# Performance work log

Hardware: AMD Instinct MI355X
Metric: run time of the kernel (lower is better)

The kernel has to match this reference:

```python
import jax, jax.numpy as jnp
from jax import lax
import numpy as np

NUM_CLASSES = 85742  # MS1M-scale classifier
C = 512              # feature channels
KH = KW = 1          # 1x1 conv classifier kernel
B = 512              # batch size
H = W = 7            # feature map spatial size


def setup_inputs() -> dict:
    key = jax.random.key(0)
    kx, kw = jax.random.split(key)
    x = jax.random.normal(kx, (B, C, H, W), dtype=jnp.float32)
    # labels: all distinct so torch's labels.unique() has deterministic size B
    labels = jnp.arange(B, dtype=jnp.int64)
    weight = jax.random.normal(kw, (NUM_CLASSES, C, KH, KW), dtype=jnp.float32) * 0.02
    bias = jnp.zeros((NUM_CLASSES,), dtype=jnp.float32)  # requires_grad=False in torch
    return {"x": x, "labels": labels, "weight": weight, "bias": bias}


def reference(x, labels, weight, bias):
    # Partial-FC style: gather the unique-label subset of the classifier weight,
    # then run a conv producing logits only over that subset.
    # jnp.unique with static size=B is jit-compatible; labels are all distinct here.
    labels_unique = jnp.unique(labels, size=labels.shape[0], fill_value=0)  # [U], sorted
    w_sub = weight[labels_unique]   # [U, C, KH, KW] irregular gather
    b_sub = bias[labels_unique]     # [U]
    logits = lax.conv_general_dilated(
        x, w_sub,
        window_strides=(1, 1), padding="VALID",
        dimension_numbers=("NCHW", "OIHW", "NCHW"),
    )  # [B, U, H, W]
    return logits + b_sub[None, :, None, None]
```

## Files before the change

kernel.cpp:

```cpp
#include <hip/hip_runtime.h>
#include <hip/hip_bf16.h>

#define CIN    512
#define BATCH  512
#define HW     49
#define UDIM   512
#define MTOT   (BATCH * HW)
#define MT     128
#define NMB    (MTOT / MT)
#define UHALF  256
#define KT     16
#define NSTEP  (CIN / KT)
#define NBLK   (NMB * 2)

typedef short  bf16x8 __attribute__((ext_vector_type(8)));
typedef short  s16x4  __attribute__((ext_vector_type(4)));
typedef float  f32x16 __attribute__((ext_vector_type(16)));

#define MFMA32(A, B, C) __builtin_amdgcn_mfma_f32_32x32x16_bf16((A), (B), (C), 0, 0, 0)

__device__ __forceinline__ void gload_lds16(const void* g, void* l) {
  __builtin_amdgcn_global_load_lds(
      (const __attribute__((address_space(1))) void*)g,
      (__attribute__((address_space(3))) void*)l, 16, 0, 0);
}

__device__ __forceinline__ void split2(float v, unsigned short& h, unsigned short& l) {
  unsigned int b  = __float_as_uint(v);
  unsigned int hb = (b + 0x7FFFu + ((b >> 16) & 1u)) >> 16;
  float hf        = __uint_as_float(hb << 16);
  unsigned int lb = __float_as_uint(v - hf);
  h = (unsigned short)hb;
  l = (unsigned short)((lb + 0x7FFFu + ((lb >> 16) & 1u)) >> 16);
}

__device__ __forceinline__ f32x16 zero16() {
  f32x16 r;
#pragma unroll
  for (int i = 0; i < 16; ++i) r[i] = 0.f;
  return r;
}

__global__ void sort_gather(const int* __restrict__ labels,
                            const float* __restrict__ bias,
                            int* __restrict__ sorted,
                            float* __restrict__ bsub)
{
  __shared__ int sl[BATCH];
  const int i = threadIdx.x;
  const int stride = (labels[1] == 0) ? 2 : 1;
  const int li = labels[i * stride];
  sl[i] = li;
  __syncthreads();
  int rank = 0;
#pragma unroll 8
  for (int j = 0; j < BATCH; ++j) rank += (sl[j] < li) ? 1 : 0;
  sorted[rank] = li;
  bsub[rank]   = bias[li];
}

__global__ void wprep(const float* __restrict__ weight,
                      const int* __restrict__ sorted,
                      unsigned short* __restrict__ whi,
                      unsigned short* __restrict__ wlo)
{
  const int u   = blockIdx.x;
  const int lbl = sorted[u];
  const float* wrow = weight + (size_t)lbl * CIN;
  for (int k = threadIdx.x; k < CIN; k += 256) {
    unsigned short h, l;
    split2(wrow[k], h, l);
    const int s = k >> 4, kq = (k >> 3) & 1, j = k & 7;
    const size_t idx = (((size_t)(s * 2 + kq)) * UDIM + u) * 8 + j;
    whi[idx] = h;
    wlo[idx] = l;
  }
}

__global__ __launch_bounds__(512, 4) void convcls_main(
    const float* __restrict__ x,
    const unsigned short* __restrict__ whi,
    const unsigned short* __restrict__ wlo,
    const float* __restrict__ bsub,
    float* __restrict__ out)
{
  __shared__ __attribute__((aligned(16))) unsigned short WhB[2][2][UHALF][8];
  __shared__ __attribute__((aligned(16))) unsigned short WlB[2][2][UHALF][8];
  __shared__ __attribute__((aligned(16))) unsigned short XhB[2][2][MT][8];
  __shared__ __attribute__((aligned(16))) unsigned short XlB[2][2][MT][8];

  const int bid = blockIdx.x;
  const int swz = (bid & 7) * (NBLK / 8) + (bid >> 3);
  const int uh  = swz / NMB;
  const int mb  = swz - uh * NMB;

  const int tid  = threadIdx.x;
  const int wave = tid >> 6, lane = tid & 63;
  const int l31  = lane & 31, lq = lane >> 5;

  const int mloc = tid & 127;
  const int ks   = tid >> 7;
  const int kqs  = ks >> 1;
  const int j0   = (ks & 1) * 4;
  const int mg   = mb * MT + mloc;
  const int bimg = mg / HW;
  const int hwp  = mg - bimg * HW;
  const float* xsrc = x + (size_t)bimg * (CIN * HW) + hwp;

  const size_t wsrcbase =
      ((size_t)(wave >> 2) * UDIM + uh * UHALF + (wave & 3) * 64) * 8 + lane * 8;

  f32x16 a00 = zero16(), a01 = zero16(), a10 = zero16(), a11 = zero16();

  const int uoff = (wave & 3) * 64;
  const int moff = (wave >> 2) * 64;

  {
    float v[4];
#pragma unroll
    for (int i = 0; i < 4; ++i) v[i] = xsrc[(size_t)(ks * 4 + i) * HW];
    gload_lds16(whi + wsrcbase, (char*)&WhB[0][0][0][0] + wave * 1024);
    gload_lds16(wlo + wsrcbase, (char*)&WlB[0][0][0][0] + wave * 1024);
    s16x4 ph, pl;
#pragma unroll
    for (int i = 0; i < 4; ++i) {
      unsigned short h, l; split2(v[i], h, l);
      ph[i] = (short)h; pl[i] = (short)l;
    }
    *(s16x4*)&XhB[0][kqs][mloc][j0] = ph;
    *(s16x4*)&XlB[0][kqs][mloc][j0] = pl;
  }
  __syncthreads();

  for (int s = 0; s < NSTEP; ++s) {
    const int cur = s & 1, nxt = cur ^ 1;
    const bool pf = (s + 1 < NSTEP);
    float v[4];
    if (pf) {
      const size_t so = (size_t)(s + 1) * (2 * UDIM * 8);
      gload_lds16(whi + so + wsrcbase, (char*)&WhB[nxt][0][0][0] + wave * 1024);
      gload_lds16(wlo + so + wsrcbase, (char*)&WlB[nxt][0][0][0] + wave * 1024);
#pragma unroll
      for (int i = 0; i < 4; ++i)
        v[i] = xsrc[(size_t)((s + 1) * KT + ks * 4 + i) * HW];
    }

    bf16x8 ah0 = *(const bf16x8*)&WhB[cur][lq][uoff + l31][0];
    bf16x8 ah1 = *(const bf16x8*)&WhB[cur][lq][uoff + 32 + l31][0];
    bf16x8 al0 = *(const bf16x8*)&WlB[cur][lq][uoff + l31][0];
    bf16x8 al1 = *(const bf16x8*)&WlB[cur][lq][uoff + 32 + l31][0];
    bf16x8 bh0 = *(const bf16x8*)&XhB[cur][lq][moff + l31][0];
    bf16x8 bh1 = *(const bf16x8*)&XhB[cur][lq][moff + 32 + l31][0];
    bf16x8 bl0 = *(const bf16x8*)&XlB[cur][lq][moff + l31][0];
    bf16x8 bl1 = *(const bf16x8*)&XlB[cur][lq][moff + 32 + l31][0];

    a00 = MFMA32(ah0, bh0, a00);  a01 = MFMA32(ah0, bh1, a01);
    a10 = MFMA32(ah1, bh0, a10);  a11 = MFMA32(ah1, bh1, a11);
    a00 = MFMA32(ah0, bl0, a00);  a01 = MFMA32(ah0, bl1, a01);
    a10 = MFMA32(ah1, bl0, a10);  a11 = MFMA32(ah1, bl1, a11);
    a00 = MFMA32(al0, bh0, a00);  a01 = MFMA32(al0, bh1, a01);
    a10 = MFMA32(al1, bh0, a10);  a11 = MFMA32(al1, bh1, a11);

    if (pf) {
      s16x4 ph, pl;
#pragma unroll
      for (int i = 0; i < 4; ++i) {
        unsigned short h, l; split2(v[i], h, l);
        ph[i] = (short)h; pl[i] = (short)l;
      }
      *(s16x4*)&XhB[nxt][kqs][mloc][j0] = ph;
      *(s16x4*)&XlB[nxt][kqs][mloc][j0] = pl;
    }
    __syncthreads();
  }

  const int u0g = uh * UHALF + uoff;
  const int m0g = mb * MT + moff;
  const int mA  = m0g + l31,      mB = m0g + 32 + l31;
  const int bA  = mA / HW,        hA = mA - bA * HW;
  const int bB  = mB / HW,        hB = mB - bB * HW;
  float* oA = out + (size_t)bA * (UDIM * HW) + hA;
  float* oB = out + (size_t)bB * (UDIM * HW) + hB;
#pragma unroll
  for (int r = 0; r < 16; ++r) {
    const int urow = (r & 3) + 8 * (r >> 2) + 4 * lq;
    {
      const int u = u0g + urow;
      const float bs = bsub[u];
      oA[(size_t)u * HW] = a00[r] + bs;
      oB[(size_t)u * HW] = a01[r] + bs;
    }
    {
      const int u = u0g + 32 + urow;
      const float bs = bsub[u];
      oA[(size_t)u * HW] = a10[r] + bs;
      oB[(size_t)u * HW] = a11[r] + bs;
    }
  }
}

extern "C" void kernel_launch(void* const* d_in, const int* in_sizes, int n_in,
                              void* d_out, int out_size, void* d_ws, size_t ws_size,
                              hipStream_t stream)
{
  const float* x      = (const float*)d_in[0];
  const int*   labels = (const int*)d_in[1];
  const float* weight = (const float*)d_in[2];
  const float* bias   = (const float*)d_in[3];
  float*       out    = (float*)d_out;

  int*            sorted = (int*)d_ws;
  float*          bsub   = (float*)((char*)d_ws + 2048);
  unsigned short* whi    = (unsigned short*)((char*)d_ws + 4096);
  unsigned short* wlo    = (unsigned short*)((char*)d_ws + 4096 + 512 * 1024);

  sort_gather<<<1, BATCH, 0, stream>>>(labels, bias, sorted, bsub);
  wprep<<<UDIM, 256, 0, stream>>>(weight, sorted, whi, wlo);
  convcls_main<<<NBLK, 512, 0, stream>>>(x, whi, wlo, bsub, out);
}
```

Measured before the change: 314.0 us.

## Fuse label sort, weight gather and split into main conv kernel

Removes the separate sort and weight-prep kernels. Each block now ranks the labels itself, gathers its half of the weight rows straight from global memory, and splits them into bf16 hi/lo inside the main loop. This saves two launches and the round trip of the prepared weights through the workspace. In exchange, every block repeats the 512x512 rank computation and the hi/lo conversion of the weights, and uses plain vector loads instead of direct-to-LDS loads.

```diff
diff --git a/kernel.cpp b/kernel.cpp
--- a/kernel.cpp
+++ b/kernel.cpp
@@ -15,15 +15,11 @@
 
 typedef short  bf16x8 __attribute__((ext_vector_type(8)));
 typedef short  s16x4  __attribute__((ext_vector_type(4)));
+typedef short  s16x8  __attribute__((ext_vector_type(8)));
+typedef float  f32x4  __attribute__((ext_vector_type(4)));
 typedef float  f32x16 __attribute__((ext_vector_type(16)));
 
 #define MFMA32(A, B, C) __builtin_amdgcn_mfma_f32_32x32x16_bf16((A), (B), (C), 0, 0, 0)
-
-__device__ __forceinline__ void gload_lds16(const void* g, void* l) {
-  __builtin_amdgcn_global_load_lds(
-      (const __attribute__((address_space(1))) void*)g,
-      (__attribute__((address_space(3))) void*)l, 16, 0, 0);
-}
 
 __device__ __forceinline__ void split2(float v, unsigned short& h, unsigned short& l) {
   unsigned int b  = __float_as_uint(v);
@@ -41,53 +37,20 @@
   return r;
 }
 
-__global__ void sort_gather(const int* __restrict__ labels,
-                            const float* __restrict__ bias,
-                            int* __restrict__ sorted,
-                            float* __restrict__ bsub)
-{
-  __shared__ int sl[BATCH];
-  const int i = threadIdx.x;
-  const int stride = (labels[1] == 0) ? 2 : 1;
-  const int li = labels[i * stride];
-  sl[i] = li;
-  __syncthreads();
-  int rank = 0;
-#pragma unroll 8
-  for (int j = 0; j < BATCH; ++j) rank += (sl[j] < li) ? 1 : 0;
-  sorted[rank] = li;
-  bsub[rank]   = bias[li];
-}
-
-__global__ void wprep(const float* __restrict__ weight,
-                      const int* __restrict__ sorted,
-                      unsigned short* __restrict__ whi,
-                      unsigned short* __restrict__ wlo)
-{
-  const int u   = blockIdx.x;
-  const int lbl = sorted[u];
-  const float* wrow = weight + (size_t)lbl * CIN;
-  for (int k = threadIdx.x; k < CIN; k += 256) {
-    unsigned short h, l;
-    split2(wrow[k], h, l);
-    const int s = k >> 4, kq = (k >> 3) & 1, j = k & 7;
-    const size_t idx = (((size_t)(s * 2 + kq)) * UDIM + u) * 8 + j;
-    whi[idx] = h;
-    wlo[idx] = l;
-  }
-}
-
-__global__ __launch_bounds__(512, 4) void convcls_main(
+__global__ __launch_bounds__(512, 4) void convcls_fused(
     const float* __restrict__ x,
-    const unsigned short* __restrict__ whi,
-    const unsigned short* __restrict__ wlo,
-    const float* __restrict__ bsub,
-    float* __restrict__ out)
+    const int*   __restrict__ labels,
+    const float* __restrict__ weight,
+    const float* __restrict__ bias,
+    float*       __restrict__ out)
 {
   __shared__ __attribute__((aligned(16))) unsigned short WhB[2][2][UHALF][8];
   __shared__ __attribute__((aligned(16))) unsigned short WlB[2][2][UHALF][8];
   __shared__ __attribute__((aligned(16))) unsigned short XhB[2][2][MT][8];
   __shared__ __attribute__((aligned(16))) unsigned short XlB[2][2][MT][8];
+  __shared__ int   sl[BATCH];
+  __shared__ int   lblr[UHALF];
+  __shared__ float bsubs[UHALF];
 
   const int bid = blockIdx.x;
   const int swz = (bid & 7) * (NBLK / 8) + (bid >> 3);
@@ -98,6 +61,22 @@
   const int wave = tid >> 6, lane = tid & 63;
   const int l31  = lane & 31, lq = lane >> 5;
 
+  {
+    const int stride = (labels[1] == 0) ? 2 : 1;
+    const int lt = labels[tid * stride];
+    sl[tid] = lt;
+    __syncthreads();
+    int rank = 0;
+#pragma unroll 8
+    for (int j = 0; j < BATCH; ++j) rank += (sl[j] < lt) ? 1 : 0;
+    const int rloc = rank - uh * UHALF;
+    if ((unsigned)rloc < UHALF) { lblr[rloc] = lt; bsubs[rloc] = bias[lt]; }
+    __syncthreads();
+  }
+
+  const int uloc = tid & 255;
+  const int kq   = tid >> 8;
+  const float* wp = weight + (size_t)lblr[uloc] * CIN + kq * 8;
   const int mloc = tid & 127;
   const int ks   = tid >> 7;
   const int kqs  = ks >> 1;
@@ -107,42 +86,48 @@
   const int hwp  = mg - bimg * HW;
   const float* xsrc = x + (size_t)bimg * (CIN * HW) + hwp;
 
-  const size_t wsrcbase =
-      ((size_t)(wave >> 2) * UDIM + uh * UHALF + (wave & 3) * 64) * 8 + lane * 8;
-
   f32x16 a00 = zero16(), a01 = zero16(), a10 = zero16(), a11 = zero16();
-
   const int uoff = (wave & 3) * 64;
   const int moff = (wave >> 2) * 64;
 
   {
-    float v[4];
-#pragma unroll
-    for (int i = 0; i < 4; ++i) v[i] = xsrc[(size_t)(ks * 4 + i) * HW];
-    gload_lds16(whi + wsrcbase, (char*)&WhB[0][0][0][0] + wave * 1024);
-    gload_lds16(wlo + wsrcbase, (char*)&WlB[0][0][0][0] + wave * 1024);
-    s16x4 ph, pl;
+    f32x4 w0 = *(const f32x4*)(wp);
+    f32x4 w1 = *(const f32x4*)(wp + 4);
+    float xv[4];
+#pragma unroll
+    for (int i = 0; i < 4; ++i) xv[i] = xsrc[(size_t)(ks * 4 + i) * HW];
+    s16x8 ph, pl;
 #pragma unroll
     for (int i = 0; i < 4; ++i) {
-      unsigned short h, l; split2(v[i], h, l);
-      ph[i] = (short)h; pl[i] = (short)l;
-    }
-    *(s16x4*)&XhB[0][kqs][mloc][j0] = ph;
-    *(s16x4*)&XlB[0][kqs][mloc][j0] = pl;
+      unsigned short h, l;
+      split2(w0[i], h, l); ph[i] = (short)h;     pl[i] = (short)l;
+      split2(w1[i], h, l); ph[4 + i] = (short)h; pl[4 + i] = (short)l;
+    }
+    *(s16x8*)&WhB[0][kq][uloc][0] = ph;
+    *(s16x8*)&WlB[0][kq][uloc][0] = pl;
+    s16x4 qh, ql;
+#pragma unroll
+    for (int i = 0; i < 4; ++i) {
+      unsigned short h, l; split2(xv[i], h, l);
+      qh[i] = (short)h; ql[i] = (short)l;
+    }
+    *(s16x4*)&XhB[0][kqs][mloc][j0] = qh;
+    *(s16x4*)&XlB[0][kqs][mloc][j0] = ql;
   }
   __syncthreads();
 
   for (int s = 0; s < NSTEP; ++s) {
     const int cur = s & 1, nxt = cur ^ 1;
     const bool pf = (s + 1 < NSTEP);
-    float v[4];
+    f32x4 w0, w1;
+    float xv[4];
     if (pf) {
-      const size_t so = (size_t)(s + 1) * (2 * UDIM * 8);
-      gload_lds16(whi + so + wsrcbase, (char*)&WhB[nxt][0][0][0] + wave * 1024);
-      gload_lds16(wlo + so + wsrcbase, (char*)&WlB[nxt][0][0][0] + wave * 1024);
-#pragma unroll
-      for (int i = 0; i < 4; ++i)
-        v[i] = xsrc[(size_t)((s + 1) * KT + ks * 4 + i) * HW];
+      const float* wps = wp + (size_t)(s + 1) * KT;
+      w0 = *(const f32x4*)(wps);
+      w1 = *(const f32x4*)(wps + 4);
+      const float* xs = xsrc + (size_t)(s + 1) * KT * HW;
+#pragma unroll
+      for (int i = 0; i < 4; ++i) xv[i] = xs[(size_t)(ks * 4 + i) * HW];
     }
 
     bf16x8 ah0 = *(const bf16x8*)&WhB[cur][lq][uoff + l31][0];
@@ -162,14 +147,23 @@
     a10 = MFMA32(al1, bh0, a10);  a11 = MFMA32(al1, bh1, a11);
 
     if (pf) {
-      s16x4 ph, pl;
+      s16x8 ph, pl;
 #pragma unroll
       for (int i = 0; i < 4; ++i) {
-        unsigned short h, l; split2(v[i], h, l);
-        ph[i] = (short)h; pl[i] = (short)l;
+        unsigned short h, l;
+        split2(w0[i], h, l); ph[i] = (short)h;     pl[i] = (short)l;
+        split2(w1[i], h, l); ph[4 + i] = (short)h; pl[4 + i] = (short)l;
       }
-      *(s16x4*)&XhB[nxt][kqs][mloc][j0] = ph;
-      *(s16x4*)&XlB[nxt][kqs][mloc][j0] = pl;
+      *(s16x8*)&WhB[nxt][kq][uloc][0] = ph;
+      *(s16x8*)&WlB[nxt][kq][uloc][0] = pl;
+      s16x4 qh, ql;
+#pragma unroll
+      for (int i = 0; i < 4; ++i) {
+        unsigned short h, l; split2(xv[i], h, l);
+        qh[i] = (short)h; ql[i] = (short)l;
+      }
+      *(s16x4*)&XhB[nxt][kqs][mloc][j0] = qh;
+      *(s16x4*)&XlB[nxt][kqs][mloc][j0] = ql;
     }
     __syncthreads();
   }
@@ -185,14 +179,16 @@
   for (int r = 0; r < 16; ++r) {
     const int urow = (r & 3) + 8 * (r >> 2) + 4 * lq;
     {
+      const int ul = uoff + urow;
+      const float bs = bsubs[ul];
       const int u = u0g + urow;
-      const float bs = bsub[u];
       oA[(size_t)u * HW] = a00[r] + bs;
       oB[(size_t)u * HW] = a01[r] + bs;
     }
     {
+      const int ul = uoff + 32 + urow;
+      const float bs = bsubs[ul];
       const int u = u0g + 32 + urow;
-      const float bs = bsub[u];
       oA[(size_t)u * HW] = a10[r] + bs;
       oB[(size_t)u * HW] = a11[r] + bs;
     }
@@ -209,12 +205,5 @@
   const float* bias   = (const float*)d_in[3];
   float*       out    = (float*)d_out;
 
-  int*            sorted = (int*)d_ws;
-  float*          bsub   = (float*)((char*)d_ws + 2048);
-  unsigned short* whi    = (unsigned short*)((char*)d_ws + 4096);
-  unsigned short* wlo    = (unsigned short*)((char*)d_ws + 4096 + 512 * 1024);
-
-  sort_gather<<<1, BATCH, 0, stream>>>(labels, bias, sorted, bsub);
-  wprep<<<UDIM, 256, 0, stream>>>(weight, sorted, whi, wlo);
-  convcls_main<<<NBLK, 512, 0, stream>>>(x, whi, wlo, bsub, out);
-}
+  convcls_fused<<<NBLK, 512, 0, stream>>>(x, labels, weight, bias, out);
+}
```

Measured after the change: 328.4 us. +4.6%, slower.
